# Performance work log

Measured on AMD Instinct MI355X. Metric: run time of the kernel, lower is better.

Reference implementation:

```python
import jax, jax.numpy as jnp
import numpy as np

N, M, D = 32768, 8192, 256


def setup_inputs() -> dict:
    key = jax.random.key(0)
    kx, ky = jax.random.split(key)
    inputDataX = jax.random.normal(kx, (N, D), dtype=jnp.float32)
    targetDataY = jax.random.normal(ky, (M, D), dtype=jnp.float32)
    dualVariablePsi = jnp.zeros((M,), dtype=jnp.float32)
    return {"inputDataX": inputDataX, "targetDataY": targetDataY, "dualVariablePsi": dualVariablePsi}


def reference(inputDataX, targetDataY, dualVariablePsi):
    # cost[i,j] = 0.5 * ||x_i - y_j||^2, built GEMM-style as in the torch module
    sq_x = jnp.sum(inputDataX ** 2, axis=1, keepdims=True)          # [N, 1]
    sq_y = jnp.sum(targetDataY ** 2, axis=1)[None, :]               # [1, M]
    cross = inputDataX @ targetDataY.T                              # [N, M]
    cost = (sq_x + sq_y - 2.0 * cross) * 0.5
    row_min = jnp.min(cost - dualVariablePsi[None, :], axis=1)      # [N]
    n = inputDataX.shape[0]
    return jnp.sum(row_min) / n + jnp.mean(dualVariablePsi)
```

## Files before the change

kernel.cpp:

```cpp
#include <hip/hip_runtime.h>
#include <hip/hip_bf16.h>
#include <stdint.h>

#define NROWS 32768
#define MCOLS 8192
#define DDIM  256

#define BM 128
#define BN 64
#define NT (MCOLS/BN)
#define NWG (NROWS/BM)

typedef __attribute__((ext_vector_type(8))) int   int8v;
typedef __attribute__((ext_vector_type(4))) int   int4v;
typedef __attribute__((ext_vector_type(4))) float f32x4;

#define AS1 __attribute__((address_space(1)))
#define AS3 __attribute__((address_space(3)))

#define CS_OFF 65536
#define RW_OFF 98304

__device__ __forceinline__ uint32_t pk4_fp8(float4 v) {
  int p = __builtin_amdgcn_cvt_pk_fp8_f32(v.x, v.y, 0, false);
  p = __builtin_amdgcn_cvt_pk_fp8_f32(v.z, v.w, p, true);
  return (uint32_t)p;
}
__device__ __forceinline__ f32x4 vmin4(f32x4 x, f32x4 y) {
  f32x4 r;
  r[0] = fminf(x[0], y[0]); r[1] = fminf(x[1], y[1]);
  r[2] = fminf(x[2], y[2]); r[3] = fminf(x[3], y[3]);
  return r;
}

__global__ void k_prep(const float* __restrict__ X, const float* __restrict__ Y,
                       const float* __restrict__ psi,
                       uint32_t* __restrict__ XqN, uint32_t* __restrict__ Yq,
                       float* __restrict__ xhalf, float* __restrict__ cbuf,
                       float* __restrict__ sum_accum)
{
  const int lane = threadIdx.x & 63;
  const int gw = (blockIdx.x * blockDim.x + threadIdx.x) >> 6;
  const int nw = (gridDim.x * blockDim.x) >> 6;
  for (int row = gw; row < NROWS + MCOLS; row += nw) {
    const bool isX = row < NROWS;
    const int r = isX ? row : row - NROWS;
    const float* src = isX ? (X + (size_t)row * DDIM) : (Y + (size_t)r * DDIM);
    float4 v = ((const float4*)src)[lane];
    const uint32_t pk = pk4_fp8(v);
    if (isX) XqN[(size_t)row * 64 + lane] = pk ^ 0x80808080u;
    else     Yq[(size_t)r * 64 + lane] = pk;
    float s = v.x*v.x + v.y*v.y + v.z*v.z + v.w*v.w;
    #pragma unroll
    for (int m = 32; m >= 1; m >>= 1) s += __shfl_xor(s, m);
    if (lane == 0) {
      if (isX) xhalf[row] = 0.5f * s;
      else     cbuf[r] = 0.5f * s - psi[r];
    }
  }
  if (blockIdx.x == 0 && threadIdx.x == 0) sum_accum[0] = 0.0f;
}

#define STAGE(t_, h_) do {                                                      \
    _Pragma("unroll") for (int _g = 0; _g < 4; ++_g)                            \
      __builtin_amdgcn_global_load_lds(                                         \
          (const AS1 uint32_t*)(srcG[_g] + (size_t)(t_) * 16384),               \
          (AS3 uint32_t*)(ldsB + wbase + (h_) + _g * 1024), 16, 0, 0);          \
  } while (0)

#define ITERC(t_, h_, ACC) do {                                                 \
    asm volatile("s_waitcnt vmcnt(4)" ::: "memory");                            \
    int8v bf0, bf1;                                                             \
    {                                                                           \
      const char* _b = ldsB + wbase + (h_) + c15 * 256;                         \
      const int4v _l0 = *(const int4v*)(_b + (((w4 * 2 + 0) ^ c15) << 4));      \
      const int4v _h0 = *(const int4v*)(_b + (((w4 * 2 + 1) ^ c15) << 4));      \
      const int4v _l1 = *(const int4v*)(_b + (((8 + w4 * 2 + 0) ^ c15) << 4));  \
      const int4v _h1 = *(const int4v*)(_b + (((8 + w4 * 2 + 1) ^ c15) << 4));  \
      bf0 = (int8v){_l0[0],_l0[1],_l0[2],_l0[3],_h0[0],_h0[1],_h0[2],_h0[3]};   \
      bf1 = (int8v){_l1[0],_l1[1],_l1[2],_l1[3],_h1[0],_h1[1],_h1[2],_h1[3]};   \
    }                                                                           \
    const float cj = *(const float*)(ldsB + CS_OFF + (((t_) * 64) << 2) + cjo); \
    const f32x4 _ci = {cj, cj, cj, cj};                                         \
    _Pragma("unroll") for (int _m = 0; _m < 4; ++_m)                            \
      ACC[_m] = __builtin_amdgcn_mfma_scale_f32_16x16x128_f8f6f4(               \
          a[_m][0], bf0, _ci, 0, 0, 0, 0x7F, 0, 0x7F);                          \
    _Pragma("unroll") for (int _m = 0; _m < 4; ++_m)                            \
      ACC[_m] = __builtin_amdgcn_mfma_scale_f32_16x16x128_f8f6f4(               \
          a[_m][1], bf1, ACC[_m], 0, 0, 0, 0x7F, 0, 0x7F);                      \
    __builtin_amdgcn_sched_barrier(0);                                          \
    if ((t_) + 2 < NT) STAGE((t_) + 2, h_);                                     \
  } while (0)

__global__ __attribute__((amdgpu_flat_work_group_size(512, 512),
                          amdgpu_waves_per_eu(2, 2)))
void k_gemm(const uint32_t* __restrict__ XqN, const uint32_t* __restrict__ Yq,
            const float* __restrict__ cbuf, const float* __restrict__ xhalf,
            float* __restrict__ sum_accum)
{
  __shared__ __align__(16) char ldsB[100352 + 8];

  const int brow = blockIdx.x * BM;
  const int tid  = threadIdx.x;
  const int wid  = tid >> 6;
  const int lane = tid & 63;
  const int rg    = wid >> 2;
  const int strip = wid & 3;
  const int c15 = lane & 15;
  const int w4  = lane >> 4;
  const int wbase = wid * 8192;
  const int cjo = (strip * 16 + c15) << 2;

  int8v a[4][2];
  {
    const char* aBase = (const char*)XqN + ((size_t)(brow + rg * 64 + c15) << 8) + w4 * 32;
    #pragma unroll
    for (int m = 0; m < 4; ++m)
      #pragma unroll
      for (int kc = 0; kc < 2; ++kc)
        a[m][kc] = *(const int8v*)(aBase + m * 4096 + kc * 128);
  }

  const char* srcG[4];
  #pragma unroll
  for (int g = 0; g < 4; ++g) {
    const int cin = 4 * g + (lane >> 4);
    const int col = strip * 16 + cin;
    srcG[g] = (const char*)Yq + (size_t)col * 256 + (((lane & 15) ^ (cin & 15)) << 4);
  }

  #pragma unroll
  for (int g = 0; g < 4; ++g)
    __builtin_amdgcn_global_load_lds(
        (const AS1 uint32_t*)((const char*)cbuf + wid * 4096 + g * 1024 + lane * 16),
        (AS3 uint32_t*)(ldsB + CS_OFF + wid * 4096 + g * 1024), 16, 0, 0);
  STAGE(0, 0);
  STAGE(1, 4096);
  asm volatile("s_waitcnt vmcnt(0)" ::: "memory");
  __builtin_amdgcn_s_barrier();

  f32x4 vmin[4];
  #pragma unroll
  for (int m = 0; m < 4; ++m)
    vmin[m] = (f32x4){3.4e38f, 3.4e38f, 3.4e38f, 3.4e38f};

  #pragma unroll 1
  for (int tt = 0; tt < NT; tt += 2) {
    f32x4 accP[4], accQ[4];
    ITERC(tt,     0,    accP);
    ITERC(tt + 1, 4096, accQ);
    #pragma unroll
    for (int m = 0; m < 4; ++m)
      vmin[m] = vmin4(vmin4(vmin[m], accP[m]), accQ[m]);
  }

  float* Rw = (float*)(ldsB + RW_OFF);
  #pragma unroll
  for (int m = 0; m < 4; ++m) {
    #pragma unroll
    for (int r = 0; r < 4; ++r) {
      float v = vmin[m][r];
      v = fminf(v, __shfl_xor(v, 1));
      v = fminf(v, __shfl_xor(v, 2));
      v = fminf(v, __shfl_xor(v, 4));
      v = fminf(v, __shfl_xor(v, 8));
      vmin[m][r] = v;
    }
    if (c15 < 4) {
      float vsel = vmin[m][0];
      vsel = (c15 == 1) ? vmin[m][1] : vsel;
      vsel = (c15 == 2) ? vmin[m][2] : vsel;
      vsel = (c15 == 3) ? vmin[m][3] : vsel;
      Rw[strip * 128 + rg * 64 + m * 16 + w4 * 4 + c15] = vsel;
    }
  }
  __syncthreads();

  float* part = (float*)(ldsB + 100352);
  if (tid < BM) {
    float rm = fminf(fminf(Rw[tid], Rw[128 + tid]),
                     fminf(Rw[256 + tid], Rw[384 + tid]));
    float s = rm + xhalf[brow + tid];
    #pragma unroll
    for (int m = 32; m >= 1; m >>= 1) s += __shfl_xor(s, m);
    if (lane == 0) part[wid] = s;
  }
  __syncthreads();
  if (tid == 0) atomicAdd(sum_accum, part[0] + part[1]);
}

__global__ void k_final(const float* __restrict__ psi, const float* __restrict__ sum_accum,
                        float* __restrict__ out)
{
  __shared__ float sh[4];
  float s = 0.f;
  for (int i = threadIdx.x; i < MCOLS; i += 256) s += psi[i];
  #pragma unroll
  for (int m = 32; m >= 1; m >>= 1) s += __shfl_xor(s, m);
  const int wid = threadIdx.x >> 6, lane = threadIdx.x & 63;
  if (lane == 0) sh[wid] = s;
  __syncthreads();
  if (threadIdx.x == 0)
    out[0] = sum_accum[0] / (float)NROWS + (sh[0] + sh[1] + sh[2] + sh[3]) / (float)MCOLS;
}

extern "C" void kernel_launch(void* const* d_in, const int* in_sizes, int n_in,
                              void* d_out, int out_size, void* d_ws, size_t ws_size,
                              hipStream_t stream)
{
  const float* X   = (const float*)d_in[0];
  const float* Y   = (const float*)d_in[1];
  const float* psi = (const float*)d_in[2];
  float* out = (float*)d_out;

  char* ws = (char*)d_ws;
  uint32_t* XqN    = (uint32_t*)(ws);
  uint32_t* Yq     = (uint32_t*)(ws + (size_t)NROWS * DDIM);
  float* cbuf      = (float*)(ws + (size_t)(NROWS + MCOLS) * DDIM);
  float* xhalf     = (float*)((char*)cbuf + (size_t)MCOLS * 4);
  float* sum_accum = (float*)((char*)xhalf + (size_t)NROWS * 4);

  k_prep <<<2048, 256, 0, stream>>>(X, Y, psi, XqN, Yq, xhalf, cbuf, sum_accum);
  k_gemm <<<NWG, 512, 0, stream>>>(XqN, Yq, cbuf, xhalf, sum_accum);
  k_final<<<1, 256, 0, stream>>>(psi, sum_accum, out);
}
```

Baseline: 77.88 us.

## Fuse X quantization into GEMM and fold final reduction via ticket

The X fp8 quantization and row-norm computation move from the prep kernel into the GEMM kernel's A-fragment load, so the quantized copy of X is no longer written to and re-read from global memory. The prep kernel now handles only Y plus the psi mean. The separate final kernel is replaced by a last-block-done ticket atomic inside the GEMM kernel, which removes one launch. The per-tile cj LDS loads are also prefetched one iteration ahead. In exchange, the GEMM prologue reads fp32 X directly (twice the bytes) and converts it in registers, which could raise register pressure.

After: 96.46 us. 23.9% more time.

```diff
diff --git a/kernel.cpp b/kernel.cpp
--- a/kernel.cpp
+++ b/kernel.cpp
@@ -18,8 +18,10 @@
 #define AS1 __attribute__((address_space(1)))
 #define AS3 __attribute__((address_space(3)))
 
-#define CS_OFF 65536
-#define RW_OFF 98304
+#define CS_OFF   65536
+#define RW_OFF   98304
+#define PART_OFF 100352
+#define XH_OFF   100368
 
 __device__ __forceinline__ uint32_t pk4_fp8(float4 v) {
   int p = __builtin_amdgcn_cvt_pk_fp8_f32(v.x, v.y, 0, false);
@@ -33,32 +35,36 @@
   return r;
 }
 
-__global__ void k_prep(const float* __restrict__ X, const float* __restrict__ Y,
-                       const float* __restrict__ psi,
-                       uint32_t* __restrict__ XqN, uint32_t* __restrict__ Yq,
-                       float* __restrict__ xhalf, float* __restrict__ cbuf,
-                       float* __restrict__ sum_accum)
+__global__ void k_prepY(const float* __restrict__ Y, const float* __restrict__ psi,
+                        uint32_t* __restrict__ Yq, float* __restrict__ cbuf,
+                        float* __restrict__ psum, float* __restrict__ sum_accum,
+                        uint32_t* __restrict__ ticket)
 {
+  if (blockIdx.x == 0) {
+    __shared__ float sh[4];
+    float s = 0.f;
+    for (int i = threadIdx.x; i < MCOLS; i += 256) s += psi[i];
+    #pragma unroll
+    for (int m = 32; m >= 1; m >>= 1) s += __shfl_xor(s, m);
+    if ((threadIdx.x & 63) == 0) sh[threadIdx.x >> 6] = s;
+    __syncthreads();
+    if (threadIdx.x == 0) {
+      psum[0] = (sh[0] + sh[1] + sh[2] + sh[3]) / (float)MCOLS;
+      sum_accum[0] = 0.0f;
+      ticket[0] = 0u;
+    }
+  }
   const int lane = threadIdx.x & 63;
   const int gw = (blockIdx.x * blockDim.x + threadIdx.x) >> 6;
   const int nw = (gridDim.x * blockDim.x) >> 6;
-  for (int row = gw; row < NROWS + MCOLS; row += nw) {
-    const bool isX = row < NROWS;
-    const int r = isX ? row : row - NROWS;
-    const float* src = isX ? (X + (size_t)row * DDIM) : (Y + (size_t)r * DDIM);
-    float4 v = ((const float4*)src)[lane];
-    const uint32_t pk = pk4_fp8(v);
-    if (isX) XqN[(size_t)row * 64 + lane] = pk ^ 0x80808080u;
-    else     Yq[(size_t)r * 64 + lane] = pk;
+  for (int r = gw; r < MCOLS; r += nw) {
+    float4 v = ((const float4*)(Y + (size_t)r * DDIM))[lane];
+    Yq[(size_t)r * 64 + lane] = pk4_fp8(v);
     float s = v.x*v.x + v.y*v.y + v.z*v.z + v.w*v.w;
     #pragma unroll
     for (int m = 32; m >= 1; m >>= 1) s += __shfl_xor(s, m);
-    if (lane == 0) {
-      if (isX) xhalf[row] = 0.5f * s;
-      else     cbuf[r] = 0.5f * s - psi[r];
-    }
-  }
-  if (blockIdx.x == 0 && threadIdx.x == 0) sum_accum[0] = 0.0f;
+    if (lane == 0) cbuf[r] = 0.5f * s - psi[r];
+  }
 }
 
 #define STAGE(t_, h_) do {                                                      \
@@ -68,7 +74,7 @@
           (AS3 uint32_t*)(ldsB + wbase + (h_) + _g * 1024), 16, 0, 0);          \
   } while (0)
 
-#define ITERC(t_, h_, ACC) do {                                                 \
+#define ITERC(t_, h_, ACC, cjv) do {                                            \
     asm volatile("s_waitcnt vmcnt(4)" ::: "memory");                            \
     int8v bf0, bf1;                                                             \
     {                                                                           \
@@ -80,8 +86,7 @@
       bf0 = (int8v){_l0[0],_l0[1],_l0[2],_l0[3],_h0[0],_h0[1],_h0[2],_h0[3]};   \
       bf1 = (int8v){_l1[0],_l1[1],_l1[2],_l1[3],_h1[0],_h1[1],_h1[2],_h1[3]};   \
     }                                                                           \
-    const float cj = *(const float*)(ldsB + CS_OFF + (((t_) * 64) << 2) + cjo); \
-    const f32x4 _ci = {cj, cj, cj, cj};                                         \
+    const f32x4 _ci = {cjv, cjv, cjv, cjv};                                     \
     _Pragma("unroll") for (int _m = 0; _m < 4; ++_m)                            \
       ACC[_m] = __builtin_amdgcn_mfma_scale_f32_16x16x128_f8f6f4(               \
           a[_m][0], bf0, _ci, 0, 0, 0, 0x7F, 0, 0x7F);                          \
@@ -94,11 +99,12 @@
 
 __global__ __attribute__((amdgpu_flat_work_group_size(512, 512),
                           amdgpu_waves_per_eu(2, 2)))
-void k_gemm(const uint32_t* __restrict__ XqN, const uint32_t* __restrict__ Yq,
-            const float* __restrict__ cbuf, const float* __restrict__ xhalf,
-            float* __restrict__ sum_accum)
+void k_gemm(const float* __restrict__ X, const uint32_t* __restrict__ Yq,
+            const float* __restrict__ cbuf, const float* __restrict__ psum,
+            float* __restrict__ sum_accum, uint32_t* __restrict__ ticket,
+            float* __restrict__ out)
 {
-  __shared__ __align__(16) char ldsB[100352 + 8];
+  __shared__ __align__(16) char ldsB[XH_OFF + 512];
 
   const int brow = blockIdx.x * BM;
   const int tid  = threadIdx.x;
@@ -110,15 +116,31 @@
   const int w4  = lane >> 4;
   const int wbase = wid * 8192;
   const int cjo = (strip * 16 + c15) << 2;
+  float* xhh = (float*)(ldsB + XH_OFF);
 
   int8v a[4][2];
   {
-    const char* aBase = (const char*)XqN + ((size_t)(brow + rg * 64 + c15) << 8) + w4 * 32;
-    #pragma unroll
-    for (int m = 0; m < 4; ++m)
+    #pragma unroll
+    for (int m = 0; m < 4; ++m) {
+      float ss = 0.f;
       #pragma unroll
-      for (int kc = 0; kc < 2; ++kc)
-        a[m][kc] = *(const int8v*)(aBase + m * 4096 + kc * 128);
+      for (int kc = 0; kc < 2; ++kc) {
+        const float* xp = X + (size_t)(brow + rg * 64 + m * 16 + c15) * DDIM
+                          + kc * 128 + w4 * 32;
+        uint32_t pk8[8];
+        #pragma unroll
+        for (int q = 0; q < 8; ++q) {
+          float4 v = ((const float4*)xp)[q];
+          ss += v.x*v.x + v.y*v.y + v.z*v.z + v.w*v.w;
+          pk8[q] = pk4_fp8(v) ^ 0x80808080u;
+        }
+        a[m][kc] = (int8v){(int)pk8[0],(int)pk8[1],(int)pk8[2],(int)pk8[3],
+                           (int)pk8[4],(int)pk8[5],(int)pk8[6],(int)pk8[7]};
+      }
+      ss += __shfl_xor(ss, 16);
+      ss += __shfl_xor(ss, 32);
+      if (w4 == 0) xhh[rg * 64 + m * 16 + c15] = 0.5f * ss;
+    }
   }
 
   const char* srcG[4];
@@ -139,6 +161,9 @@
   asm volatile("s_waitcnt vmcnt(0)" ::: "memory");
   __builtin_amdgcn_s_barrier();
 
+  float cjP = *(const float*)(ldsB + CS_OFF + cjo);
+  float cjQ = *(const float*)(ldsB + CS_OFF + (64 << 2) + cjo);
+
   f32x4 vmin[4];
   #pragma unroll
   for (int m = 0; m < 4; ++m)
@@ -147,11 +172,17 @@
   #pragma unroll 1
   for (int tt = 0; tt < NT; tt += 2) {
     f32x4 accP[4], accQ[4];
-    ITERC(tt,     0,    accP);
-    ITERC(tt + 1, 4096, accQ);
+    ITERC(tt, 0, accP, cjP);
+    float cjP2 = 0.f, cjQ2 = 0.f;
+    if (tt + 2 < NT) {
+      cjP2 = *(const float*)(ldsB + CS_OFF + (((tt + 2) * 64) << 2) + cjo);
+      cjQ2 = *(const float*)(ldsB + CS_OFF + (((tt + 3) * 64) << 2) + cjo);
+    }
+    ITERC(tt + 1, 4096, accQ, cjQ);
     #pragma unroll
     for (int m = 0; m < 4; ++m)
       vmin[m] = vmin4(vmin4(vmin[m], accP[m]), accQ[m]);
+    cjP = cjP2; cjQ = cjQ2;
   }
 
   float* Rw = (float*)(ldsB + RW_OFF);
@@ -176,32 +207,24 @@
   }
   __syncthreads();
 
-  float* part = (float*)(ldsB + 100352);
+  float* part = (float*)(ldsB + PART_OFF);
   if (tid < BM) {
     float rm = fminf(fminf(Rw[tid], Rw[128 + tid]),
                      fminf(Rw[256 + tid], Rw[384 + tid]));
-    float s = rm + xhalf[brow + tid];
+    float s = rm + xhh[tid];
     #pragma unroll
     for (int m = 32; m >= 1; m >>= 1) s += __shfl_xor(s, m);
     if (lane == 0) part[wid] = s;
   }
   __syncthreads();
-  if (tid == 0) atomicAdd(sum_accum, part[0] + part[1]);
-}
-
-__global__ void k_final(const float* __restrict__ psi, const float* __restrict__ sum_accum,
-                        float* __restrict__ out)
-{
-  __shared__ float sh[4];
-  float s = 0.f;
-  for (int i = threadIdx.x; i < MCOLS; i += 256) s += psi[i];
-  #pragma unroll
-  for (int m = 32; m >= 1; m >>= 1) s += __shfl_xor(s, m);
-  const int wid = threadIdx.x >> 6, lane = threadIdx.x & 63;
-  if (lane == 0) sh[wid] = s;
-  __syncthreads();
-  if (threadIdx.x == 0)
-    out[0] = sum_accum[0] / (float)NROWS + (sh[0] + sh[1] + sh[2] + sh[3]) / (float)MCOLS;
+  if (tid == 0) {
+    atomicAdd(sum_accum, part[0] + part[1]);
+    __threadfence();
+    if (atomicAdd(ticket, 1u) == NWG - 1) {
+      const float tot = *(volatile float*)sum_accum;
+      out[0] = tot / (float)NROWS + psum[0];
+    }
+  }
 }
 
 extern "C" void kernel_launch(void* const* d_in, const int* in_sizes, int n_in,
@@ -214,13 +237,12 @@
   float* out = (float*)d_out;
 
   char* ws = (char*)d_ws;
-  uint32_t* XqN    = (uint32_t*)(ws);
-  uint32_t* Yq     = (uint32_t*)(ws + (size_t)NROWS * DDIM);
-  float* cbuf      = (float*)(ws + (size_t)(NROWS + MCOLS) * DDIM);
-  float* xhalf     = (float*)((char*)cbuf + (size_t)MCOLS * 4);
-  float* sum_accum = (float*)((char*)xhalf + (size_t)NROWS * 4);
-
-  k_prep <<<2048, 256, 0, stream>>>(X, Y, psi, XqN, Yq, xhalf, cbuf, sum_accum);
-  k_gemm <<<NWG, 512, 0, stream>>>(XqN, Yq, cbuf, xhalf, sum_accum);
-  k_final<<<1, 256, 0, stream>>>(psi, sum_accum, out);
-}
+  uint32_t* Yq     = (uint32_t*)(ws);
+  float* cbuf      = (float*)(ws + (size_t)MCOLS * DDIM);
+  float* psum      = (float*)((char*)cbuf + (size_t)MCOLS * 4);
+  float* sum_accum = (float*)((char*)psum + 16);
+  uint32_t* ticket = (uint32_t*)((char*)sum_accum + 16);
+
+  k_prepY<<<128, 256, 0, stream>>>(Y, psi, Yq, cbuf, psum, sum_accum, ticket);
+  k_gemm <<<NWG, 512, 0, stream>>>(X, Yq, cbuf, psum, sum_accum, ticket, out);
+}
```

## Widen column tile to 128 and keep per-column bias in registers

Applied to the files above, without the earlier changes.

Each wave now covers 32 columns per tile instead of 16, issuing two interleaved independent MFMA chains per step. The loop runs half as many iterations and folds the min update into each step. The per-column bias is now loaded straight from global memory into rotating registers rather than staged through LDS, which removes the startup block barrier. The last two iterations are peeled with explicit vmcnt values. The cost is a larger per-wave LDS staging area (about 133 KB total) and more outstanding loads per wave.

Result: no change. 79.31 us (+1.8%).

```diff
diff --git a/kernel.cpp b/kernel.cpp
--- a/kernel.cpp
+++ b/kernel.cpp
@@ -7,7 +7,7 @@
 #define DDIM  256
 
 #define BM 128
-#define BN 64
+#define BN 128
 #define NT (MCOLS/BN)
 #define NWG (NROWS/BM)
 
@@ -18,8 +18,8 @@
 #define AS1 __attribute__((address_space(1)))
 #define AS3 __attribute__((address_space(3)))
 
-#define CS_OFF 65536
-#define RW_OFF 98304
+#define RW_OFF   131072
+#define PART_OFF 133120
 
 __device__ __forceinline__ uint32_t pk4_fp8(float4 v) {
   int p = __builtin_amdgcn_cvt_pk_fp8_f32(v.x, v.y, 0, false);
@@ -62,34 +62,49 @@
 }
 
 #define STAGE(t_, h_) do {                                                      \
-    _Pragma("unroll") for (int _g = 0; _g < 4; ++_g)                            \
+    _Pragma("unroll") for (int _g = 0; _g < 8; ++_g)                            \
       __builtin_amdgcn_global_load_lds(                                         \
-          (const AS1 uint32_t*)(srcG[_g] + (size_t)(t_) * 16384),               \
+          (const AS1 uint32_t*)(srcG[_g] + (size_t)(t_) * 32768),               \
           (AS3 uint32_t*)(ldsB + wbase + (h_) + _g * 1024), 16, 0, 0);          \
   } while (0)
 
-#define ITERC(t_, h_, ACC) do {                                                 \
-    asm volatile("s_waitcnt vmcnt(4)" ::: "memory");                            \
-    int8v bf0, bf1;                                                             \
+#define ITERC(t_, h_, VM, ISSUE) do {                                           \
+    asm volatile("s_waitcnt " VM ::: "memory");                                 \
+    int8v bf0[2], bf1[2];                                                       \
     {                                                                           \
       const char* _b = ldsB + wbase + (h_) + c15 * 256;                         \
-      const int4v _l0 = *(const int4v*)(_b + (((w4 * 2 + 0) ^ c15) << 4));      \
-      const int4v _h0 = *(const int4v*)(_b + (((w4 * 2 + 1) ^ c15) << 4));      \
-      const int4v _l1 = *(const int4v*)(_b + (((8 + w4 * 2 + 0) ^ c15) << 4));  \
-      const int4v _h1 = *(const int4v*)(_b + (((8 + w4 * 2 + 1) ^ c15) << 4));  \
-      bf0 = (int8v){_l0[0],_l0[1],_l0[2],_l0[3],_h0[0],_h0[1],_h0[2],_h0[3]};   \
-      bf1 = (int8v){_l1[0],_l1[1],_l1[2],_l1[3],_h1[0],_h1[1],_h1[2],_h1[3]};   \
-    }                                                                           \
-    const float cj = *(const float*)(ldsB + CS_OFF + (((t_) * 64) << 2) + cjo); \
-    const f32x4 _ci = {cj, cj, cj, cj};                                         \
+      _Pragma("unroll") for (int _kc = 0; _kc < 2; ++_kc) {                     \
+        const int4v _l0 = *(const int4v*)(_b + (((_kc*8 + w4*2 + 0) ^ c15) << 4)); \
+        const int4v _h0 = *(const int4v*)(_b + (((_kc*8 + w4*2 + 1) ^ c15) << 4)); \
+        const int4v _l1 = *(const int4v*)(_b + 4096 + (((_kc*8 + w4*2 + 0) ^ c15) << 4)); \
+        const int4v _h1 = *(const int4v*)(_b + 4096 + (((_kc*8 + w4*2 + 1) ^ c15) << 4)); \
+        bf0[_kc] = (int8v){_l0[0],_l0[1],_l0[2],_l0[3],_h0[0],_h0[1],_h0[2],_h0[3]}; \
+        bf1[_kc] = (int8v){_l1[0],_l1[1],_l1[2],_l1[3],_h1[0],_h1[1],_h1[2],_h1[3]}; \
+      }                                                                         \
+    }                                                                           \
+    const f32x4 _c0 = {cj0, cj0, cj0, cj0};                                     \
+    const f32x4 _c1 = {cj1, cj1, cj1, cj1};                                     \
+    f32x4 acc0[4], acc1[4];                                                     \
+    _Pragma("unroll") for (int _m = 0; _m < 4; ++_m) {                          \
+      acc0[_m] = __builtin_amdgcn_mfma_scale_f32_16x16x128_f8f6f4(              \
+          a[_m][0], bf0[0], _c0, 0, 0, 0, 0x7F, 0, 0x7F);                       \
+      acc1[_m] = __builtin_amdgcn_mfma_scale_f32_16x16x128_f8f6f4(              \
+          a[_m][0], bf1[0], _c1, 0, 0, 0, 0x7F, 0, 0x7F);                       \
+    }                                                                           \
+    _Pragma("unroll") for (int _m = 0; _m < 4; ++_m) {                          \
+      acc0[_m] = __builtin_amdgcn_mfma_scale_f32_16x16x128_f8f6f4(              \
+          a[_m][1], bf0[1], acc0[_m], 0, 0, 0, 0x7F, 0, 0x7F);                  \
+      acc1[_m] = __builtin_amdgcn_mfma_scale_f32_16x16x128_f8f6f4(              \
+          a[_m][1], bf1[1], acc1[_m], 0, 0, 0, 0x7F, 0, 0x7F);                  \
+    }                                                                           \
+    __builtin_amdgcn_sched_barrier(0);                                          \
+    if (ISSUE) {                                                                \
+      cj0 = cjPtr[((t_) + 2) * BN];                                             \
+      cj1 = cjPtr[((t_) + 2) * BN + 16];                                        \
+      STAGE((t_) + 2, h_);                                                      \
+    }                                                                           \
     _Pragma("unroll") for (int _m = 0; _m < 4; ++_m)                            \
-      ACC[_m] = __builtin_amdgcn_mfma_scale_f32_16x16x128_f8f6f4(               \
-          a[_m][0], bf0, _ci, 0, 0, 0, 0x7F, 0, 0x7F);                          \
-    _Pragma("unroll") for (int _m = 0; _m < 4; ++_m)                            \
-      ACC[_m] = __builtin_amdgcn_mfma_scale_f32_16x16x128_f8f6f4(               \
-          a[_m][1], bf1, ACC[_m], 0, 0, 0, 0x7F, 0, 0x7F);                      \
-    __builtin_amdgcn_sched_barrier(0);                                          \
-    if ((t_) + 2 < NT) STAGE((t_) + 2, h_);                                     \
+      vmin[_m] = vmin4(vmin4(vmin[_m], acc0[_m]), acc1[_m]);                    \
   } while (0)
 
 __global__ __attribute__((amdgpu_flat_work_group_size(512, 512),
@@ -98,7 +113,7 @@
             const float* __restrict__ cbuf, const float* __restrict__ xhalf,
             float* __restrict__ sum_accum)
 {
-  __shared__ __align__(16) char ldsB[100352 + 8];
+  __shared__ __align__(16) char ldsB[PART_OFF + 16];
 
   const int brow = blockIdx.x * BM;
   const int tid  = threadIdx.x;
@@ -108,8 +123,7 @@
   const int strip = wid & 3;
   const int c15 = lane & 15;
   const int w4  = lane >> 4;
-  const int wbase = wid * 8192;
-  const int cjo = (strip * 16 + c15) << 2;
+  const int wbase = wid * 16384;
 
   int8v a[4][2];
   {
@@ -121,23 +135,19 @@
         a[m][kc] = *(const int8v*)(aBase + m * 4096 + kc * 128);
   }
 
-  const char* srcG[4];
-  #pragma unroll
-  for (int g = 0; g < 4; ++g) {
+  const char* srcG[8];
+  #pragma unroll
+  for (int g = 0; g < 8; ++g) {
     const int cin = 4 * g + (lane >> 4);
-    const int col = strip * 16 + cin;
+    const int col = strip * 32 + cin;
     srcG[g] = (const char*)Yq + (size_t)col * 256 + (((lane & 15) ^ (cin & 15)) << 4);
   }
-
-  #pragma unroll
-  for (int g = 0; g < 4; ++g)
-    __builtin_amdgcn_global_load_lds(
-        (const AS1 uint32_t*)((const char*)cbuf + wid * 4096 + g * 1024 + lane * 16),
-        (AS3 uint32_t*)(ldsB + CS_OFF + wid * 4096 + g * 1024), 16, 0, 0);
+  const float* cjPtr = cbuf + strip * 32 + c15;
+
+  float cj0 = cjPtr[0], cj1 = cjPtr[16];
   STAGE(0, 0);
-  STAGE(1, 4096);
-  asm volatile("s_waitcnt vmcnt(0)" ::: "memory");
-  __builtin_amdgcn_s_barrier();
+  float cjN0 = cjPtr[BN], cjN1 = cjPtr[BN + 16];
+  STAGE(1, 8192);
 
   f32x4 vmin[4];
   #pragma unroll
@@ -145,14 +155,15 @@
     vmin[m] = (f32x4){3.4e38f, 3.4e38f, 3.4e38f, 3.4e38f};
 
   #pragma unroll 1
-  for (int tt = 0; tt < NT; tt += 2) {
-    f32x4 accP[4], accQ[4];
-    ITERC(tt,     0,    accP);
-    ITERC(tt + 1, 4096, accQ);
-    #pragma unroll
-    for (int m = 0; m < 4; ++m)
-      vmin[m] = vmin4(vmin4(vmin[m], accP[m]), accQ[m]);
-  }
+  for (int tt = 0; tt < NT - 2; tt += 2) {
+    ITERC(tt, 0, "vmcnt(10)", 1);
+    { float t0 = cj0, t1 = cj1; cj0 = cjN0; cj1 = cjN1; cjN0 = t0; cjN1 = t1; }
+    ITERC(tt + 1, 8192, "vmcnt(10)", 1);
+    { float t0 = cj0, t1 = cj1; cj0 = cjN0; cj1 = cjN1; cjN0 = t0; cjN1 = t1; }
+  }
+  ITERC(NT - 2, 0, "vmcnt(10)", 0);
+  { float t0 = cj0, t1 = cj1; cj0 = cjN0; cj1 = cjN1; cjN0 = t0; cjN1 = t1; }
+  ITERC(NT - 1, 8192, "vmcnt(0)", 0);
 
   float* Rw = (float*)(ldsB + RW_OFF);
   #pragma unroll
@@ -176,7 +187,7 @@
   }
   __syncthreads();
 
-  float* part = (float*)(ldsB + 100352);
+  float* part = (float*)(ldsB + PART_OFF);
   if (tid < BM) {
     float rm = fminf(fminf(Rw[tid], Rw[128 + tid]),
                      fminf(Rw[256 + tid], Rw[384 + tid]));
```
